# Kernel optimization log

Measured on AMD Instinct MI355X. Metric: run time of the kernel, lower is better.

## Reference

```python
import jax, jax.numpy as jnp
import numpy as np

T_GRID = 2048  # static grid size (= density * data range 128)
EPS = 1e-8


def rbf(x1, x2, ls, os_):
    # x1: [B,N,1], x2: [B,M,1] -> [B,N,M]; gpytorch ScaleKernel(RBFKernel())
    d2 = (x1 - jnp.swapaxes(x2, -1, -2)) ** 2
    return os_ * jnp.exp(-0.5 * d2 / (ls * ls))


def conv1d(x, w, b):
    # x: [B,C,T], w: [O,I,5], pad 2 -> same length
    y = jax.lax.conv_general_dilated(x, w, (1,), [(2, 2)],
                                     dimension_numbers=('NCH', 'OIH', 'NCH'))
    return y + b[None, :, None]


def setup_inputs() -> dict:
    key = jax.random.key(0)
    ks = jax.random.split(key, 12)
    B, Nc, Nt = 16, 2048, 2048
    xc = jax.random.uniform(ks[0], (B, Nc, 1), jnp.float32) * 128.0
    yc = jax.random.normal(ks[1], (B, Nc, 1), jnp.float32)
    xt = jax.random.uniform(ks[2], (B, Nt, 1), jnp.float32) * 128.0
    ln2 = float(np.log(2.0))  # softplus(0), gpytorch default raw param init
    params = {
        'ls_psi': jnp.float32(ln2), 'os_psi': jnp.float32(ln2),
        'ls_rho': jnp.float32(ln2), 'os_rho': jnp.float32(ln2),
        'w1': jax.random.normal(ks[3], (16, 3, 5), jnp.float32) * 0.2,
        'b1': jnp.zeros((16,), jnp.float32),
        'w2': jax.random.normal(ks[4], (32, 16, 5), jnp.float32) * 0.1,
        'b2': jnp.zeros((32,), jnp.float32),
        'w3': jax.random.normal(ks[5], (16, 32, 5), jnp.float32) * 0.1,
        'b3': jnp.zeros((16,), jnp.float32),
        'w4': jax.random.normal(ks[6], (2, 16, 5), jnp.float32) * 0.1,
        'b4': jnp.zeros((2,), jnp.float32),
    }
    return {'xc': xc, 'yc': yc, 'xt': xt, **params}


def reference(xc, yc, xt, ls_psi, os_psi, ls_rho, os_rho,
              w1, b1, w2, b2, w3, b3, w4, b4):
    B = xc.shape[0]
    lower = jnp.minimum(xc.min(), xt.min())
    upper = jnp.maximum(xc.max(), xt.max())
    t = jnp.linspace(lower, upper, T_GRID)                      # [T]
    t = jnp.broadcast_to(t[None, :, None], (B, T_GRID, 1))      # [B,T,1]

    # SetConv encoder: h = psi(t, xc) @ phi(yc), phi = [y^0, y^1]
    Kt = rbf(t, xc, ls_psi, os_psi)                             # [B,T,Nc]
    phi = jnp.concatenate([jnp.ones_like(yc), yc], -1)          # [B,Nc,2]
    h = jnp.matmul(Kt, phi)                                     # [B,T,2]
    h0, h1 = h[..., :1], h[..., 1:]
    h1 = h1 / (h0 + EPS)
    rep = jnp.concatenate([t, h0, h1], -1).swapaxes(-1, -2)     # [B,3,T]

    # small Conv1d decoder stack
    f = jax.nn.relu(conv1d(rep, w1, b1))
    f = jax.nn.relu(conv1d(f, w2, b2))
    f = jax.nn.relu(conv1d(f, w3, b3))
    f = conv1d(f, w4, b4).swapaxes(-1, -2)                      # [B,T,2]
    f_mu, f_sigma = f[..., :1], f[..., 1:]

    # SetConv decoder onto targets
    Kr = rbf(xt, t, ls_rho, os_rho)                             # [B,Nt,T]
    mu = jnp.matmul(Kr, f_mu)                                   # [B,Nt,1]
    sigma = jnp.matmul(Kr, jax.nn.softplus(f_sigma))            # [B,Nt,1]
    return jnp.concatenate([mu, sigma], -1)                     # [B,Nt,2]
```

## Files before the change

### kernel.cpp

```cpp
#include <hip/hip_runtime.h>
#include <math.h>

#define T_GRID 2048
#define NC 2048
#define NT 2048
#define BATCH 16
#define XCUT 28.0f
#define TILE 128
#define SW 144
#define W 149
#define PCAP 768
#define NSB 32

__global__ __launch_bounds__(1024) void k_minmax(const float4* __restrict__ xc4,
                                                 const float4* __restrict__ xt4,
                                                 float* __restrict__ mm) {
    float4 va[8], vb[8];
    int tid = threadIdx.x;
#pragma unroll
    for (int k = 0; k < 8; k++) va[k] = xc4[tid + 1024 * k];
#pragma unroll
    for (int k = 0; k < 8; k++) vb[k] = xt4[tid + 1024 * k];
    float lo = 3.4e38f, hi = -3.4e38f;
#pragma unroll
    for (int k = 0; k < 8; k++) {
        lo = fminf(lo, fminf(fminf(va[k].x, va[k].y), fminf(va[k].z, va[k].w)));
        hi = fmaxf(hi, fmaxf(fmaxf(va[k].x, va[k].y), fmaxf(va[k].z, va[k].w)));
        lo = fminf(lo, fminf(fminf(vb[k].x, vb[k].y), fminf(vb[k].z, vb[k].w)));
        hi = fmaxf(hi, fmaxf(fmaxf(vb[k].x, vb[k].y), fmaxf(vb[k].z, vb[k].w)));
    }
    for (int off = 32; off; off >>= 1) {
        lo = fminf(lo, __shfl_down(lo, off));
        hi = fmaxf(hi, __shfl_down(hi, off));
    }
    __shared__ float slo[16], shi[16];
    int lane = tid & 63, wv = tid >> 6;
    if (lane == 0) { slo[wv] = lo; shi[wv] = hi; }
    __syncthreads();
    if (tid == 0) {
        for (int w = 1; w < 16; w++) { lo = fminf(lo, slo[w]); hi = fmaxf(hi, shi[w]); }
        mm[0] = lo; mm[1] = hi;
    }
}

__global__ __launch_bounds__(576) void k_fused(
        const float* __restrict__ xc, const float* __restrict__ yc,
        const float* __restrict__ ls_psi, const float* __restrict__ os_psi,
        const float* __restrict__ mm,
        const float* __restrict__ w1, const float* __restrict__ b1,
        const float* __restrict__ w2, const float* __restrict__ b2,
        const float* __restrict__ w3, const float* __restrict__ b3,
        const float* __restrict__ w4, const float* __restrict__ b4,
        float* __restrict__ f) {
    __shared__ float rep[3][W];
    __shared__ float L1s[16][W];
    __shared__ __align__(16) char pool[32 * W * 4];
    __shared__ float w1L[15][16];
    __shared__ float w2L[80][32];
    __shared__ float w3L[160][16];
    __shared__ float w4L[80][2];
    __shared__ float bL[66];

    float (*L2s)[W] = reinterpret_cast<float (*)[W]>(pool);
    float (*L3s)[W] = L1s;
    float*  px     = reinterpret_cast<float*>(pool);
    float*  py     = reinterpret_cast<float*>(pool + 3072);
    float2* part   = reinterpret_cast<float2*>(pool + 6144);
    int*    bstart = reinterpret_cast<int*>(pool + 10752);
    int*    curi   = reinterpret_cast<int*>(pool + 10896);

    int tid = threadIdx.x;
    int b = blockIdx.y;
    int gstart = blockIdx.x * TILE - 8;

    for (int idx = tid; idx < 240; idx += 576)  { int o = idx / 15,  r2 = idx % 15;  w1L[r2][o] = w1[idx]; }
    for (int idx = tid; idx < 2560; idx += 576) { int o = idx / 80,  r2 = idx % 80;  w2L[r2][o] = w2[idx]; }
    for (int idx = tid; idx < 2560; idx += 576) { int o = idx / 160, r2 = idx % 160; w3L[r2][o] = w3[idx]; }
    for (int idx = tid; idx < 160; idx += 576)  { int o = idx / 80,  r2 = idx % 80;  w4L[r2][o] = w4[idx]; }
    if (tid < 16) bL[tid] = b1[tid];
    if (tid < 32) bL[16 + tid] = b2[tid];
    if (tid < 16) bL[48 + tid] = b3[tid];
    if (tid < 2)  bL[64 + tid] = b4[tid];
    if (tid < 4) {
        int c = (tid < 2) ? tid : tid + SW;
        for (int r2 = 0; r2 < 3; r2++)  rep[r2][c] = 0.f;
        for (int r2 = 0; r2 < 16; r2++) L1s[r2][c] = 0.f;
    }

    float lower = mm[0], upper = mm[1];
    float step = (upper - lower) * (1.0f / (T_GRID - 1));
    float ls = ls_psi[0], os = os_psi[0];
    float c2 = -0.72134752044f / (ls * ls);
    float R = ls * sqrtf(XCUT);

    int g0 = max(gstart, 0), g1 = min(gstart + SW - 1, T_GRID - 1);
    float tmin = fmaf((float)g0, step, lower) - R;
    float tmax = fmaf((float)g1, step, lower) + R;
    float sbw_inv = (float)NSB / (tmax - tmin);

    if (tid < NSB + 1) bstart[tid] = 0;
    __syncthreads();
    float xv[4], yv[4];
    int bn[4];
    const float* xb = xc + b * NC;
    const float* yb = yc + b * NC;
#pragma unroll
    for (int k = 0; k < 4; k++) {
        int idx = tid + 576 * k;
        bn[k] = -1;
        if (idx < NC) {
            xv[k] = xb[idx];
            yv[k] = yb[idx];
            if ((xv[k] >= tmin) & (xv[k] <= tmax)) {
                bn[k] = min(NSB - 1, max(0, (int)((xv[k] - tmin) * sbw_inv)));
                atomicAdd(&bstart[bn[k]], 1);
            }
        }
    }
    __syncthreads();
    if (tid == 0) {
        int run = 0;
        for (int i = 0; i < NSB; i++) { int c = bstart[i]; bstart[i] = run; run += c; }
        bstart[NSB] = run;
    }
    __syncthreads();
    if (tid < NSB) curi[tid] = bstart[tid];
    __syncthreads();
#pragma unroll
    for (int k = 0; k < 4; k++) {
        if (bn[k] >= 0) {
            int pos = atomicAdd(&curi[bn[k]], 1);
            if (pos < PCAP) { px[pos] = xv[k]; py[pos] = yv[k]; }
        }
    }
    __syncthreads();

    {
        int p = tid >> 2, rr = tid & 3;
        int gp = gstart + p;
        bool pvalid = (gp >= 0 && gp < T_GRID);
        float t = fmaf((float)gp, step, lower);
        int s = 0, e = 0;
        if (pvalid) {
            int b0 = min(NSB - 1, max(0, (int)((t - R - tmin) * sbw_inv)));
            int b1 = min(NSB - 1, max(0, (int)((t + R - tmin) * sbw_inv)));
            s = bstart[b0];
            e = min(bstart[b1 + 1], PCAP);
        }
        float S0 = 0.f, S1 = 0.f;
        for (int j = s + rr; j < e; j += 4) {
            float xj = px[j], yj = py[j];
            float d = t - xj;
            float ev = exp2f(d * d * c2);
            S0 += ev;
            S1 = fmaf(ev, yj, S1);
        }
        part[rr * SW + p] = make_float2(S0, S1);
        __syncthreads();
        if (tid < SW) {
            float2 q0 = part[tid], q1 = part[tid + SW], q2 = part[tid + 2 * SW], q3 = part[tid + 3 * SW];
            float T0 = q0.x + q1.x + q2.x + q3.x;
            float T1 = q0.y + q1.y + q2.y + q3.y;
            int gp2 = gstart + tid;
            bool pv2 = (gp2 >= 0 && gp2 < T_GRID);
            float h0 = os * T0;
            float h1 = os * T1 / (h0 + 1e-8f);
            rep[0][tid + 2] = pv2 ? fmaf((float)gp2, step, lower) : 0.f;
            rep[1][tid + 2] = pv2 ? h0 : 0.f;
            rep[2][tid + 2] = pv2 ? h1 : 0.f;
        }
    }
    __syncthreads();

    {
        if (tid < 4) {
            int c = (tid < 2) ? tid : tid + SW;
            for (int r2 = 0; r2 < 32; r2++) L2s[r2][c] = 0.f;
        }
        int o = tid & 15, s0 = (tid >> 4) << 2;
        float acc[4];
        float bias = bL[o];
#pragma unroll
        for (int s = 0; s < 4; s++) acc[s] = bias;
        for (int i = 0; i < 3; i++) {
            float x[8];
#pragma unroll
            for (int j = 0; j < 8; j++) x[j] = rep[i][s0 + j];
#pragma unroll
            for (int k = 0; k < 5; k++) {
                float w = w1L[i * 5 + k][o];
#pragma unroll
                for (int s = 0; s < 4; s++) acc[s] = fmaf(x[s + k], w, acc[s]);
            }
        }
#pragma unroll
        for (int s = 0; s < 4; s++) {
            int p = s0 + s, gp = gstart + p;
            bool vv = (p >= 2 && p < SW - 2 && gp >= 0 && gp < T_GRID);
            L1s[o][p + 2] = vv ? fmaxf(acc[s], 0.f) : 0.f;
        }
    }
    __syncthreads();

    {
        int o = tid & 31, s0 = (tid >> 5) << 3;
        float acc[8];
        float bias = bL[16 + o];
#pragma unroll
        for (int s = 0; s < 8; s++) acc[s] = bias;
        for (int i = 0; i < 16; i++) {
            float x[12];
#pragma unroll
            for (int j = 0; j < 12; j++) x[j] = L1s[i][s0 + j];
#pragma unroll
            for (int k = 0; k < 5; k++) {
                float w = w2L[i * 5 + k][o];
#pragma unroll
                for (int s = 0; s < 8; s++) acc[s] = fmaf(x[s + k], w, acc[s]);
            }
        }
#pragma unroll
        for (int s = 0; s < 8; s++) {
            int p = s0 + s, gp = gstart + p;
            bool vv = (p >= 4 && p < SW - 4 && gp >= 0 && gp < T_GRID);
            L2s[o][p + 2] = vv ? fmaxf(acc[s], 0.f) : 0.f;
        }
    }
    __syncthreads();

    {
        int o = tid & 15, s0 = (tid >> 4) << 2;
        float acc[4];
        float bias = bL[48 + o];
#pragma unroll
        for (int s = 0; s < 4; s++) acc[s] = bias;
        for (int i = 0; i < 32; i++) {
            float x[8];
#pragma unroll
            for (int j = 0; j < 8; j++) x[j] = L2s[i][s0 + j];
#pragma unroll
            for (int k = 0; k < 5; k++) {
                float w = w3L[i * 5 + k][o];
#pragma unroll
                for (int s = 0; s < 4; s++) acc[s] = fmaf(x[s + k], w, acc[s]);
            }
        }
#pragma unroll
        for (int s = 0; s < 4; s++) {
            int p = s0 + s, gp = gstart + p;
            bool vv = (p >= 6 && p < SW - 6 && gp >= 0 && gp < T_GRID);
            L3s[o][p + 2] = vv ? fmaxf(acc[s], 0.f) : 0.f;
        }
    }
    __syncthreads();

    if (tid < 256) {
        int o = tid & 1, po = tid >> 1;
        float a = bL[64 + o];
        for (int i = 0; i < 16; i++) {
#pragma unroll
            for (int k = 0; k < 5; k++) {
                a = fmaf(L3s[i][po + 8 + k], w4L[i * 5 + k][o], a);
            }
        }
        int gp = blockIdx.x * TILE + po;
        if (o) {
            float sp = fmaxf(a, 0.f) + log1pf(expf(-fabsf(a)));
            f[2 * (b * T_GRID + gp) + 1] = sp;
        } else {
            f[2 * (b * T_GRID + gp)] = a;
        }
    }
}

__global__ __launch_bounds__(256) void k_out(const float* __restrict__ xt,
                                             const float* __restrict__ ls_rho,
                                             const float* __restrict__ os_rho,
                                             const float* __restrict__ mm,
                                             const float2* __restrict__ f,
                                             float2* __restrict__ out) {
    __shared__ float smx[T_GRID];
    __shared__ float ssg[T_GRID];
    __shared__ float2 part[256];
    int b = blockIdx.y, tid = threadIdx.x;
    int it = blockIdx.x * 64 + (tid & 63);
    int r = tid >> 6;
    float lower = mm[0], upper = mm[1];
    float step = (upper - lower) * (1.0f / (T_GRID - 1));
    float invstep = 1.0f / step;
    float ls = ls_rho[0], os = os_rho[0];
    float c2 = -0.72134752044f / (ls * ls);
    float R = ls * sqrtf(XCUT);
    float x = xt[b * NT + it];

    const float2* fb = f + b * T_GRID;
    for (int k = tid; k < T_GRID; k += 256) {
        float2 v = fb[k];
        smx[k] = v.x; ssg[k] = v.y;
    }
    __syncthreads();

    int j0 = max(0, (int)floorf((x - R - lower) * invstep));
    int j1 = min(T_GRID - 1, (int)ceilf((x + R - lower) * invstep));

    float Smu = 0.f, Ssg = 0.f;
    float jf = (float)(j0 + r);
    for (int j = j0 + r; j <= j1; j += 4) {
        float d = x - fmaf(jf, step, lower);
        float e = exp2f(d * d * c2);
        Smu = fmaf(e, smx[j], Smu);
        Ssg = fmaf(e, ssg[j], Ssg);
        jf += 4.0f;
    }
    part[tid] = make_float2(Smu, Ssg);
    __syncthreads();
    if (r == 0) {
#pragma unroll
        for (int q = 64; q < 256; q += 64) {
            float2 pp = part[tid + q];
            Smu += pp.x; Ssg += pp.y;
        }
        out[b * NT + it] = make_float2(os * Smu, os * Ssg);
    }
}

extern "C" void kernel_launch(void* const* d_in, const int* in_sizes, int n_in,
                              void* d_out, int out_size, void* d_ws, size_t ws_size,
                              hipStream_t stream) {
    const float* xc = (const float*)d_in[0];
    const float* yc = (const float*)d_in[1];
    const float* xt = (const float*)d_in[2];
    const float* ls_psi = (const float*)d_in[3];
    const float* os_psi = (const float*)d_in[4];
    const float* ls_rho = (const float*)d_in[5];
    const float* os_rho = (const float*)d_in[6];
    const float* w1 = (const float*)d_in[7];
    const float* b1 = (const float*)d_in[8];
    const float* w2 = (const float*)d_in[9];
    const float* b2 = (const float*)d_in[10];
    const float* w3 = (const float*)d_in[11];
    const float* b3 = (const float*)d_in[12];
    const float* w4 = (const float*)d_in[13];
    const float* b4 = (const float*)d_in[14];

    char* ws = (char*)d_ws;
    float* mm = (float*)ws;
    float* f  = (float*)(ws + 64);

    k_minmax<<<dim3(1), dim3(1024), 0, stream>>>((const float4*)xc, (const float4*)xt, mm);

    k_fused<<<dim3(T_GRID / TILE, BATCH), dim3(576), 0, stream>>>(
        xc, yc, ls_psi, os_psi, mm,
        w1, b1, w2, b2, w3, b3, w4, b4, f);

    k_out<<<dim3(NT / 64, BATCH), dim3(256), 0, stream>>>(
        xt, ls_rho, os_rho, mm, (const float2*)f, (float2*)d_out);
}
```

Baseline: 109.6 us.

## Fuse all three kernels into one persistent kernel with grid barriers

Replaces the min/max, fused encoder+conv, and output kernels with a single 256-block kernel that uses software grid barriers on a workspace counter. The min/max is distributed across blocks with atomicMin/Max on order-preserving mapped floats, and the output stage reuses the same blocks with 512 active threads. This removes two kernel launch gaps and the serial single-block reduction, at the risk of barrier spin overhead and reliance on all 256 blocks being co-resident.

```diff
diff --git a/kernel.cpp b/kernel.cpp
--- a/kernel.cpp
+++ b/kernel.cpp
@@ -11,47 +11,40 @@
 #define W 149
 #define PCAP 768
 #define NSB 32
-
-__global__ __launch_bounds__(1024) void k_minmax(const float4* __restrict__ xc4,
-                                                 const float4* __restrict__ xt4,
-                                                 float* __restrict__ mm) {
-    float4 va[8], vb[8];
-    int tid = threadIdx.x;
-#pragma unroll
-    for (int k = 0; k < 8; k++) va[k] = xc4[tid + 1024 * k];
-#pragma unroll
-    for (int k = 0; k < 8; k++) vb[k] = xt4[tid + 1024 * k];
-    float lo = 3.4e38f, hi = -3.4e38f;
-#pragma unroll
-    for (int k = 0; k < 8; k++) {
-        lo = fminf(lo, fminf(fminf(va[k].x, va[k].y), fminf(va[k].z, va[k].w)));
-        hi = fmaxf(hi, fmaxf(fmaxf(va[k].x, va[k].y), fmaxf(va[k].z, va[k].w)));
-        lo = fminf(lo, fminf(fminf(vb[k].x, vb[k].y), fminf(vb[k].z, vb[k].w)));
-        hi = fmaxf(hi, fmaxf(fmaxf(vb[k].x, vb[k].y), fmaxf(vb[k].z, vb[k].w)));
-    }
-    for (int off = 32; off; off >>= 1) {
-        lo = fminf(lo, __shfl_down(lo, off));
-        hi = fmaxf(hi, __shfl_down(hi, off));
-    }
-    __shared__ float slo[16], shi[16];
-    int lane = tid & 63, wv = tid >> 6;
-    if (lane == 0) { slo[wv] = lo; shi[wv] = hi; }
+#define NBLK 256u
+#define MAGIC 0x1234ABCDu
+
+__device__ __forceinline__ unsigned mapf(float x) {
+    unsigned b = __float_as_uint(x);
+    return (b & 0x80000000u) ? ~b : (b | 0x80000000u);
+}
+__device__ __forceinline__ float unmapf(unsigned u) {
+    return (u & 0x80000000u) ? __uint_as_float(u & 0x7fffffffu) : __uint_as_float(~u);
+}
+
+__device__ __forceinline__ void gbar(unsigned* ctr) {
     __syncthreads();
-    if (tid == 0) {
-        for (int w = 1; w < 16; w++) { lo = fminf(lo, slo[w]); hi = fmaxf(hi, shi[w]); }
-        mm[0] = lo; mm[1] = hi;
-    }
-}
-
-__global__ __launch_bounds__(576) void k_fused(
+    if (threadIdx.x == 0) {
+        __threadfence();
+        __hip_atomic_fetch_add(ctr, 1u, __ATOMIC_RELEASE, __HIP_MEMORY_SCOPE_AGENT);
+        while (__hip_atomic_load(ctr, __ATOMIC_ACQUIRE, __HIP_MEMORY_SCOPE_AGENT) < NBLK)
+            __builtin_amdgcn_s_sleep(1);
+        __threadfence();
+    }
+    __syncthreads();
+}
+
+__global__ __launch_bounds__(576) void k_all(
         const float* __restrict__ xc, const float* __restrict__ yc,
+        const float* __restrict__ xt,
         const float* __restrict__ ls_psi, const float* __restrict__ os_psi,
-        const float* __restrict__ mm,
+        const float* __restrict__ ls_rho, const float* __restrict__ os_rho,
         const float* __restrict__ w1, const float* __restrict__ b1,
         const float* __restrict__ w2, const float* __restrict__ b2,
         const float* __restrict__ w3, const float* __restrict__ b3,
         const float* __restrict__ w4, const float* __restrict__ b4,
-        float* __restrict__ f) {
+        unsigned* __restrict__ syncv, float* __restrict__ f,
+        float2* __restrict__ out) {
     __shared__ float rep[3][W];
     __shared__ float L1s[16][W];
     __shared__ __align__(16) char pool[32 * W * 4];
@@ -70,8 +63,10 @@
     int*    curi   = reinterpret_cast<int*>(pool + 10896);
 
     int tid = threadIdx.x;
-    int b = blockIdx.y;
-    int gstart = blockIdx.x * TILE - 8;
+    int bid = blockIdx.x;
+    int b = bid >> 4;
+    int j = bid & 15;
+    int gstart = j * TILE - 8;
 
     for (int idx = tid; idx < 240; idx += 576)  { int o = idx / 15,  r2 = idx % 15;  w1L[r2][o] = w1[idx]; }
     for (int idx = tid; idx < 2560; idx += 576) { int o = idx / 80,  r2 = idx % 80;  w2L[r2][o] = w2[idx]; }
@@ -87,241 +82,276 @@
         for (int r2 = 0; r2 < 16; r2++) L1s[r2][c] = 0.f;
     }
 
-    float lower = mm[0], upper = mm[1];
+    float lo = 3.4e38f, hi = -3.4e38f;
+    if (tid < 64) {
+        const float4* p4 = (tid < 32) ? ((const float4*)xc + bid * 32 + tid)
+                                      : ((const float4*)xt + bid * 32 + (tid - 32));
+        float4 v = *p4;
+        lo = fminf(fminf(v.x, v.y), fminf(v.z, v.w));
+        hi = fmaxf(fmaxf(v.x, v.y), fmaxf(v.z, v.w));
+    }
+
+    if (tid == 0) {
+        if (bid == 0) {
+            __hip_atomic_store(&syncv[1], 0u, __ATOMIC_RELAXED, __HIP_MEMORY_SCOPE_AGENT);
+            __hip_atomic_store(&syncv[2], 0u, __ATOMIC_RELAXED, __HIP_MEMORY_SCOPE_AGENT);
+            __hip_atomic_store(&syncv[3], 0u, __ATOMIC_RELAXED, __HIP_MEMORY_SCOPE_AGENT);
+            __hip_atomic_store(&syncv[4], 0xFFFFFFFFu, __ATOMIC_RELAXED, __HIP_MEMORY_SCOPE_AGENT);
+            __hip_atomic_store(&syncv[5], 0u, __ATOMIC_RELAXED, __HIP_MEMORY_SCOPE_AGENT);
+            __hip_atomic_store(&syncv[0], MAGIC, __ATOMIC_RELEASE, __HIP_MEMORY_SCOPE_AGENT);
+        }
+        while (__hip_atomic_load(&syncv[0], __ATOMIC_ACQUIRE, __HIP_MEMORY_SCOPE_AGENT) != MAGIC)
+            __builtin_amdgcn_s_sleep(1);
+    }
+    __syncthreads();
+
+    if (tid < 64) {
+        for (int off = 32; off; off >>= 1) {
+            lo = fminf(lo, __shfl_down(lo, off));
+            hi = fmaxf(hi, __shfl_down(hi, off));
+        }
+        if (tid == 0) {
+            atomicMin(&syncv[4], mapf(lo));
+            atomicMax(&syncv[5], mapf(hi));
+        }
+    }
+    gbar(&syncv[1]);
+
+    float lower = unmapf(__hip_atomic_load(&syncv[4], __ATOMIC_RELAXED, __HIP_MEMORY_SCOPE_AGENT));
+    float upper = unmapf(__hip_atomic_load(&syncv[5], __ATOMIC_RELAXED, __HIP_MEMORY_SCOPE_AGENT));
     float step = (upper - lower) * (1.0f / (T_GRID - 1));
-    float ls = ls_psi[0], os = os_psi[0];
-    float c2 = -0.72134752044f / (ls * ls);
-    float R = ls * sqrtf(XCUT);
-
-    int g0 = max(gstart, 0), g1 = min(gstart + SW - 1, T_GRID - 1);
-    float tmin = fmaf((float)g0, step, lower) - R;
-    float tmax = fmaf((float)g1, step, lower) + R;
-    float sbw_inv = (float)NSB / (tmax - tmin);
-
-    if (tid < NSB + 1) bstart[tid] = 0;
-    __syncthreads();
-    float xv[4], yv[4];
-    int bn[4];
-    const float* xb = xc + b * NC;
-    const float* yb = yc + b * NC;
-#pragma unroll
-    for (int k = 0; k < 4; k++) {
-        int idx = tid + 576 * k;
-        bn[k] = -1;
-        if (idx < NC) {
-            xv[k] = xb[idx];
-            yv[k] = yb[idx];
-            if ((xv[k] >= tmin) & (xv[k] <= tmax)) {
-                bn[k] = min(NSB - 1, max(0, (int)((xv[k] - tmin) * sbw_inv)));
-                atomicAdd(&bstart[bn[k]], 1);
-            }
-        }
-    }
-    __syncthreads();
-    if (tid == 0) {
-        int run = 0;
-        for (int i = 0; i < NSB; i++) { int c = bstart[i]; bstart[i] = run; run += c; }
-        bstart[NSB] = run;
-    }
-    __syncthreads();
-    if (tid < NSB) curi[tid] = bstart[tid];
-    __syncthreads();
-#pragma unroll
-    for (int k = 0; k < 4; k++) {
-        if (bn[k] >= 0) {
-            int pos = atomicAdd(&curi[bn[k]], 1);
-            if (pos < PCAP) { px[pos] = xv[k]; py[pos] = yv[k]; }
-        }
-    }
-    __syncthreads();
 
     {
-        int p = tid >> 2, rr = tid & 3;
-        int gp = gstart + p;
-        bool pvalid = (gp >= 0 && gp < T_GRID);
-        float t = fmaf((float)gp, step, lower);
-        int s = 0, e = 0;
-        if (pvalid) {
-            int b0 = min(NSB - 1, max(0, (int)((t - R - tmin) * sbw_inv)));
-            int b1 = min(NSB - 1, max(0, (int)((t + R - tmin) * sbw_inv)));
-            s = bstart[b0];
-            e = min(bstart[b1 + 1], PCAP);
-        }
-        float S0 = 0.f, S1 = 0.f;
-        for (int j = s + rr; j < e; j += 4) {
-            float xj = px[j], yj = py[j];
-            float d = t - xj;
-            float ev = exp2f(d * d * c2);
-            S0 += ev;
-            S1 = fmaf(ev, yj, S1);
-        }
-        part[rr * SW + p] = make_float2(S0, S1);
-        __syncthreads();
-        if (tid < SW) {
-            float2 q0 = part[tid], q1 = part[tid + SW], q2 = part[tid + 2 * SW], q3 = part[tid + 3 * SW];
-            float T0 = q0.x + q1.x + q2.x + q3.x;
-            float T1 = q0.y + q1.y + q2.y + q3.y;
-            int gp2 = gstart + tid;
-            bool pv2 = (gp2 >= 0 && gp2 < T_GRID);
-            float h0 = os * T0;
-            float h1 = os * T1 / (h0 + 1e-8f);
-            rep[0][tid + 2] = pv2 ? fmaf((float)gp2, step, lower) : 0.f;
-            rep[1][tid + 2] = pv2 ? h0 : 0.f;
-            rep[2][tid + 2] = pv2 ? h1 : 0.f;
-        }
-    }
-    __syncthreads();
+        float ls = ls_psi[0], os = os_psi[0];
+        float c2 = -0.72134752044f / (ls * ls);
+        float R = ls * sqrtf(XCUT);
+
+        int g0 = max(gstart, 0), g1 = min(gstart + SW - 1, T_GRID - 1);
+        float tmin = fmaf((float)g0, step, lower) - R;
+        float tmax = fmaf((float)g1, step, lower) + R;
+        float sbw_inv = (float)NSB / (tmax - tmin);
+
+        if (tid < NSB + 1) bstart[tid] = 0;
+        __syncthreads();
+        float xv[4], yv[4];
+        int bn[4];
+        const float* xb = xc + b * NC;
+        const float* yb = yc + b * NC;
+#pragma unroll
+        for (int k = 0; k < 4; k++) {
+            int idx = tid + 576 * k;
+            bn[k] = -1;
+            if (idx < NC) {
+                xv[k] = xb[idx];
+                yv[k] = yb[idx];
+                if ((xv[k] >= tmin) & (xv[k] <= tmax)) {
+                    bn[k] = min(NSB - 1, max(0, (int)((xv[k] - tmin) * sbw_inv)));
+                    atomicAdd(&bstart[bn[k]], 1);
+                }
+            }
+        }
+        __syncthreads();
+        if (tid == 0) {
+            int run = 0;
+            for (int i = 0; i < NSB; i++) { int c = bstart[i]; bstart[i] = run; run += c; }
+            bstart[NSB] = run;
+        }
+        __syncthreads();
+        if (tid < NSB) curi[tid] = bstart[tid];
+        __syncthreads();
+#pragma unroll
+        for (int k = 0; k < 4; k++) {
+            if (bn[k] >= 0) {
+                int pos = atomicAdd(&curi[bn[k]], 1);
+                if (pos < PCAP) { px[pos] = xv[k]; py[pos] = yv[k]; }
+            }
+        }
+        __syncthreads();
+
+        {
+            int p = tid >> 2, rr = tid & 3;
+            int gp = gstart + p;
+            bool pvalid = (gp >= 0 && gp < T_GRID);
+            float t = fmaf((float)gp, step, lower);
+            int s = 0, e = 0;
+            if (pvalid) {
+                int b0 = min(NSB - 1, max(0, (int)((t - R - tmin) * sbw_inv)));
+                int b1i = min(NSB - 1, max(0, (int)((t + R - tmin) * sbw_inv)));
+                s = bstart[b0];
+                e = min(bstart[b1i + 1], PCAP);
+            }
+            float S0 = 0.f, S1 = 0.f;
+            for (int jj = s + rr; jj < e; jj += 4) {
+                float xj = px[jj], yj = py[jj];
+                float d = t - xj;
+                float ev = exp2f(d * d * c2);
+                S0 += ev;
+                S1 = fmaf(ev, yj, S1);
+            }
+            part[rr * SW + p] = make_float2(S0, S1);
+            __syncthreads();
+            if (tid < SW) {
+                float2 q0 = part[tid], q1 = part[tid + SW], q2 = part[tid + 2 * SW], q3 = part[tid + 3 * SW];
+                float T0 = q0.x + q1.x + q2.x + q3.x;
+                float T1 = q0.y + q1.y + q2.y + q3.y;
+                int gp2 = gstart + tid;
+                bool pv2 = (gp2 >= 0 && gp2 < T_GRID);
+                float h0 = os * T0;
+                float h1 = os * T1 / (h0 + 1e-8f);
+                rep[0][tid + 2] = pv2 ? fmaf((float)gp2, step, lower) : 0.f;
+                rep[1][tid + 2] = pv2 ? h0 : 0.f;
+                rep[2][tid + 2] = pv2 ? h1 : 0.f;
+            }
+        }
+        __syncthreads();
+
+        {
+            if (tid < 4) {
+                int c = (tid < 2) ? tid : tid + SW;
+                for (int r2 = 0; r2 < 32; r2++) L2s[r2][c] = 0.f;
+            }
+            int o = tid & 15, s0 = (tid >> 4) << 2;
+            float acc[4];
+            float bias = bL[o];
+#pragma unroll
+            for (int s = 0; s < 4; s++) acc[s] = bias;
+            for (int i = 0; i < 3; i++) {
+                float x[8];
+#pragma unroll
+                for (int jj = 0; jj < 8; jj++) x[jj] = rep[i][s0 + jj];
+#pragma unroll
+                for (int k = 0; k < 5; k++) {
+                    float w = w1L[i * 5 + k][o];
+#pragma unroll
+                    for (int s = 0; s < 4; s++) acc[s] = fmaf(x[s + k], w, acc[s]);
+                }
+            }
+#pragma unroll
+            for (int s = 0; s < 4; s++) {
+                int p = s0 + s, gp = gstart + p;
+                bool vv = (p >= 2 && p < SW - 2 && gp >= 0 && gp < T_GRID);
+                L1s[o][p + 2] = vv ? fmaxf(acc[s], 0.f) : 0.f;
+            }
+        }
+        __syncthreads();
+
+        {
+            int o = tid & 31, s0 = (tid >> 5) << 3;
+            float acc[8];
+            float bias = bL[16 + o];
+#pragma unroll
+            for (int s = 0; s < 8; s++) acc[s] = bias;
+            for (int i = 0; i < 16; i++) {
+                float x[12];
+#pragma unroll
+                for (int jj = 0; jj < 12; jj++) x[jj] = L1s[i][s0 + jj];
+#pragma unroll
+                for (int k = 0; k < 5; k++) {
+                    float w = w2L[i * 5 + k][o];
+#pragma unroll
+                    for (int s = 0; s < 8; s++) acc[s] = fmaf(x[s + k], w, acc[s]);
+                }
+            }
+#pragma unroll
+            for (int s = 0; s < 8; s++) {
+                int p = s0 + s, gp = gstart + p;
+                bool vv = (p >= 4 && p < SW - 4 && gp >= 0 && gp < T_GRID);
+                L2s[o][p + 2] = vv ? fmaxf(acc[s], 0.f) : 0.f;
+            }
+        }
+        __syncthreads();
+
+        {
+            int o = tid & 15, s0 = (tid >> 4) << 2;
+            float acc[4];
+            float bias = bL[48 + o];
+#pragma unroll
+            for (int s = 0; s < 4; s++) acc[s] = bias;
+            for (int i = 0; i < 32; i++) {
+                float x[8];
+#pragma unroll
+                for (int jj = 0; jj < 8; jj++) x[jj] = L2s[i][s0 + jj];
+#pragma unroll
+                for (int k = 0; k < 5; k++) {
+                    float w = w3L[i * 5 + k][o];
+#pragma unroll
+                    for (int s = 0; s < 4; s++) acc[s] = fmaf(x[s + k], w, acc[s]);
+                }
+            }
+#pragma unroll
+            for (int s = 0; s < 4; s++) {
+                int p = s0 + s, gp = gstart + p;
+                bool vv = (p >= 6 && p < SW - 6 && gp >= 0 && gp < T_GRID);
+                L3s[o][p + 2] = vv ? fmaxf(acc[s], 0.f) : 0.f;
+            }
+        }
+        __syncthreads();
+
+        if (tid < 256) {
+            int o = tid & 1, po = tid >> 1;
+            float a = bL[64 + o];
+            for (int i = 0; i < 16; i++) {
+#pragma unroll
+                for (int k = 0; k < 5; k++) {
+                    a = fmaf(L3s[i][po + 8 + k], w4L[i * 5 + k][o], a);
+                }
+            }
+            int gp = j * TILE + po;
+            if (o) {
+                float sp = fmaxf(a, 0.f) + log1pf(expf(-fabsf(a)));
+                f[2 * (b * T_GRID + gp) + 1] = sp;
+            } else {
+                f[2 * (b * T_GRID + gp)] = a;
+            }
+        }
+    }
+    gbar(&syncv[2]);
 
     {
-        if (tid < 4) {
-            int c = (tid < 2) ? tid : tid + SW;
-            for (int r2 = 0; r2 < 32; r2++) L2s[r2][c] = 0.f;
-        }
-        int o = tid & 15, s0 = (tid >> 4) << 2;
-        float acc[4];
-        float bias = bL[o];
-#pragma unroll
-        for (int s = 0; s < 4; s++) acc[s] = bias;
-        for (int i = 0; i < 3; i++) {
-            float x[8];
-#pragma unroll
-            for (int j = 0; j < 8; j++) x[j] = rep[i][s0 + j];
-#pragma unroll
-            for (int k = 0; k < 5; k++) {
-                float w = w1L[i * 5 + k][o];
-#pragma unroll
-                for (int s = 0; s < 4; s++) acc[s] = fmaf(x[s + k], w, acc[s]);
-            }
-        }
-#pragma unroll
-        for (int s = 0; s < 4; s++) {
-            int p = s0 + s, gp = gstart + p;
-            bool vv = (p >= 2 && p < SW - 2 && gp >= 0 && gp < T_GRID);
-            L1s[o][p + 2] = vv ? fmaxf(acc[s], 0.f) : 0.f;
-        }
-    }
-    __syncthreads();
-
-    {
-        int o = tid & 31, s0 = (tid >> 5) << 3;
-        float acc[8];
-        float bias = bL[16 + o];
-#pragma unroll
-        for (int s = 0; s < 8; s++) acc[s] = bias;
-        for (int i = 0; i < 16; i++) {
-            float x[12];
-#pragma unroll
-            for (int j = 0; j < 12; j++) x[j] = L1s[i][s0 + j];
-#pragma unroll
-            for (int k = 0; k < 5; k++) {
-                float w = w2L[i * 5 + k][o];
-#pragma unroll
-                for (int s = 0; s < 8; s++) acc[s] = fmaf(x[s + k], w, acc[s]);
-            }
-        }
-#pragma unroll
-        for (int s = 0; s < 8; s++) {
-            int p = s0 + s, gp = gstart + p;
-            bool vv = (p >= 4 && p < SW - 4 && gp >= 0 && gp < T_GRID);
-            L2s[o][p + 2] = vv ? fmaxf(acc[s], 0.f) : 0.f;
-        }
-    }
-    __syncthreads();
-
-    {
-        int o = tid & 15, s0 = (tid >> 4) << 2;
-        float acc[4];
-        float bias = bL[48 + o];
-#pragma unroll
-        for (int s = 0; s < 4; s++) acc[s] = bias;
-        for (int i = 0; i < 32; i++) {
-            float x[8];
-#pragma unroll
-            for (int j = 0; j < 8; j++) x[j] = L2s[i][s0 + j];
-#pragma unroll
-            for (int k = 0; k < 5; k++) {
-                float w = w3L[i * 5 + k][o];
-#pragma unroll
-                for (int s = 0; s < 4; s++) acc[s] = fmaf(x[s + k], w, acc[s]);
-            }
-        }
-#pragma unroll
-        for (int s = 0; s < 4; s++) {
-            int p = s0 + s, gp = gstart + p;
-            bool vv = (p >= 6 && p < SW - 6 && gp >= 0 && gp < T_GRID);
-            L3s[o][p + 2] = vv ? fmaxf(acc[s], 0.f) : 0.f;
-        }
-    }
-    __syncthreads();
-
-    if (tid < 256) {
-        int o = tid & 1, po = tid >> 1;
-        float a = bL[64 + o];
-        for (int i = 0; i < 16; i++) {
-#pragma unroll
-            for (int k = 0; k < 5; k++) {
-                a = fmaf(L3s[i][po + 8 + k], w4L[i * 5 + k][o], a);
-            }
-        }
-        int gp = blockIdx.x * TILE + po;
-        if (o) {
-            float sp = fmaxf(a, 0.f) + log1pf(expf(-fabsf(a)));
-            f[2 * (b * T_GRID + gp) + 1] = sp;
-        } else {
-            f[2 * (b * T_GRID + gp)] = a;
-        }
-    }
-}
-
-__global__ __launch_bounds__(256) void k_out(const float* __restrict__ xt,
-                                             const float* __restrict__ ls_rho,
-                                             const float* __restrict__ os_rho,
-                                             const float* __restrict__ mm,
-                                             const float2* __restrict__ f,
-                                             float2* __restrict__ out) {
-    __shared__ float smx[T_GRID];
-    __shared__ float ssg[T_GRID];
-    __shared__ float2 part[256];
-    int b = blockIdx.y, tid = threadIdx.x;
-    int it = blockIdx.x * 64 + (tid & 63);
-    int r = tid >> 6;
-    float lower = mm[0], upper = mm[1];
-    float step = (upper - lower) * (1.0f / (T_GRID - 1));
-    float invstep = 1.0f / step;
-    float ls = ls_rho[0], os = os_rho[0];
-    float c2 = -0.72134752044f / (ls * ls);
-    float R = ls * sqrtf(XCUT);
-    float x = xt[b * NT + it];
-
-    const float2* fb = f + b * T_GRID;
-    for (int k = tid; k < T_GRID; k += 256) {
-        float2 v = fb[k];
-        smx[k] = v.x; ssg[k] = v.y;
-    }
-    __syncthreads();
-
-    int j0 = max(0, (int)floorf((x - R - lower) * invstep));
-    int j1 = min(T_GRID - 1, (int)ceilf((x + R - lower) * invstep));
-
-    float Smu = 0.f, Ssg = 0.f;
-    float jf = (float)(j0 + r);
-    for (int j = j0 + r; j <= j1; j += 4) {
-        float d = x - fmaf(jf, step, lower);
-        float e = exp2f(d * d * c2);
-        Smu = fmaf(e, smx[j], Smu);
-        Ssg = fmaf(e, ssg[j], Ssg);
-        jf += 4.0f;
-    }
-    part[tid] = make_float2(Smu, Ssg);
-    __syncthreads();
-    if (r == 0) {
-#pragma unroll
-        for (int q = 64; q < 256; q += 64) {
-            float2 pp = part[tid + q];
-            Smu += pp.x; Ssg += pp.y;
-        }
-        out[b * NT + it] = make_float2(os * Smu, os * Ssg);
-    }
+        float* smx = reinterpret_cast<float*>(pool);
+        float* ssg = reinterpret_cast<float*>(pool + 8192);
+        float2* part3 = reinterpret_cast<float2*>(&L1s[0][0]);
+
+        float ls = ls_rho[0], os = os_rho[0];
+        float c2 = -0.72134752044f / (ls * ls);
+        float R = ls * sqrtf(XCUT);
+        float invstep = 1.0f / step;
+
+        const float2* fb = (const float2*)f + b * T_GRID;
+        for (int k = tid; k < T_GRID; k += 576) {
+            float2 v = fb[k];
+            smx[k] = v.x; ssg[k] = v.y;
+        }
+        __syncthreads();
+
+        float Smu = 0.f, Ssg = 0.f;
+        int q = tid >> 2, rr = tid & 3;
+        if (tid < 512) {
+            float x = xt[b * NT + j * 128 + q];
+            int j0 = max(0, (int)floorf((x - R - lower) * invstep));
+            int j1 = min(T_GRID - 1, (int)ceilf((x + R - lower) * invstep));
+            float jf = (float)(j0 + rr);
+            for (int jj = j0 + rr; jj <= j1; jj += 4) {
+                float d = x - fmaf(jf, step, lower);
+                float e = exp2f(d * d * c2);
+                Smu = fmaf(e, smx[jj], Smu);
+                Ssg = fmaf(e, ssg[jj], Ssg);
+                jf += 4.0f;
+            }
+            part3[rr * 128 + q] = make_float2(Smu, Ssg);
+        }
+        __syncthreads();
+        if (tid < 128) {
+            float2 p0 = part3[tid], p1 = part3[128 + tid], p2 = part3[256 + tid], p3 = part3[384 + tid];
+            float sm = p0.x + p1.x + p2.x + p3.x;
+            float sg = p0.y + p1.y + p2.y + p3.y;
+            out[b * NT + j * 128 + tid] = make_float2(os * sm, os * sg);
+        }
+    }
+
+    gbar(&syncv[3]);
+    if (bid == 0 && tid == 0)
+        __hip_atomic_store(&syncv[0], 0u, __ATOMIC_RELAXED, __HIP_MEMORY_SCOPE_AGENT);
 }
 
 extern "C" void kernel_launch(void* const* d_in, const int* in_sizes, int n_in,
@@ -344,15 +374,11 @@
     const float* b4 = (const float*)d_in[14];
 
     char* ws = (char*)d_ws;
-    float* mm = (float*)ws;
-    float* f  = (float*)(ws + 64);
-
-    k_minmax<<<dim3(1), dim3(1024), 0, stream>>>((const float4*)xc, (const float4*)xt, mm);
-
-    k_fused<<<dim3(T_GRID / TILE, BATCH), dim3(576), 0, stream>>>(
-        xc, yc, ls_psi, os_psi, mm,
-        w1, b1, w2, b2, w3, b3, w4, b4, f);
-
-    k_out<<<dim3(NT / 64, BATCH), dim3(256), 0, stream>>>(
-        xt, ls_rho, os_rho, mm, (const float2*)f, (float2*)d_out);
-}
+    unsigned* syncv = (unsigned*)ws;
+    float* f = (float*)(ws + 256);
+
+    k_all<<<dim3(NBLK), dim3(576), 0, stream>>>(
+        xc, yc, xt, ls_psi, os_psi, ls_rho, os_rho,
+        w1, b1, w2, b2, w3, b3, w4, b4,
+        syncv, f, (float2*)d_out);
+}
```

After: 172.4 us. +57.3%, slower.

## Fold global min/max reduction into fused kernel, drop separate minmax launch

Applied to the files above, without the earlier changes.

Removes the single-block min/max kernel and has every block of the fused kernel redundantly reduce all xc and xt values (256 KB) to get the grid bounds, with block (0,0) writing them out for the output kernel. This trades a serial one-block launch and its dependency for redundant global reads across 256 blocks, which will mostly hit in cache. It also vectorizes the per-batch xc load to float4 and loads yc only for in-range points. An extra barrier is added in the third conv layer because L3s aliases L1s.

```diff
diff --git a/kernel.cpp b/kernel.cpp
--- a/kernel.cpp
+++ b/kernel.cpp
@@ -12,46 +12,15 @@
 #define PCAP 768
 #define NSB 32
 
-__global__ __launch_bounds__(1024) void k_minmax(const float4* __restrict__ xc4,
-                                                 const float4* __restrict__ xt4,
-                                                 float* __restrict__ mm) {
-    float4 va[8], vb[8];
-    int tid = threadIdx.x;
-#pragma unroll
-    for (int k = 0; k < 8; k++) va[k] = xc4[tid + 1024 * k];
-#pragma unroll
-    for (int k = 0; k < 8; k++) vb[k] = xt4[tid + 1024 * k];
-    float lo = 3.4e38f, hi = -3.4e38f;
-#pragma unroll
-    for (int k = 0; k < 8; k++) {
-        lo = fminf(lo, fminf(fminf(va[k].x, va[k].y), fminf(va[k].z, va[k].w)));
-        hi = fmaxf(hi, fmaxf(fmaxf(va[k].x, va[k].y), fmaxf(va[k].z, va[k].w)));
-        lo = fminf(lo, fminf(fminf(vb[k].x, vb[k].y), fminf(vb[k].z, vb[k].w)));
-        hi = fmaxf(hi, fmaxf(fmaxf(vb[k].x, vb[k].y), fmaxf(vb[k].z, vb[k].w)));
-    }
-    for (int off = 32; off; off >>= 1) {
-        lo = fminf(lo, __shfl_down(lo, off));
-        hi = fmaxf(hi, __shfl_down(hi, off));
-    }
-    __shared__ float slo[16], shi[16];
-    int lane = tid & 63, wv = tid >> 6;
-    if (lane == 0) { slo[wv] = lo; shi[wv] = hi; }
-    __syncthreads();
-    if (tid == 0) {
-        for (int w = 1; w < 16; w++) { lo = fminf(lo, slo[w]); hi = fmaxf(hi, shi[w]); }
-        mm[0] = lo; mm[1] = hi;
-    }
-}
-
 __global__ __launch_bounds__(576) void k_fused(
         const float* __restrict__ xc, const float* __restrict__ yc,
+        const float4* __restrict__ xc4, const float4* __restrict__ xt4,
         const float* __restrict__ ls_psi, const float* __restrict__ os_psi,
-        const float* __restrict__ mm,
         const float* __restrict__ w1, const float* __restrict__ b1,
         const float* __restrict__ w2, const float* __restrict__ b2,
         const float* __restrict__ w3, const float* __restrict__ b3,
         const float* __restrict__ w4, const float* __restrict__ b4,
-        float* __restrict__ f) {
+        float* __restrict__ mm, float* __restrict__ f) {
     __shared__ float rep[3][W];
     __shared__ float L1s[16][W];
     __shared__ __align__(16) char pool[32 * W * 4];
@@ -60,6 +29,7 @@
     __shared__ float w3L[160][16];
     __shared__ float w4L[80][2];
     __shared__ float bL[66];
+    __shared__ float slo[9], shi[9];
 
     float (*L2s)[W] = reinterpret_cast<float (*)[W]>(pool);
     float (*L3s)[W] = L1s;
@@ -87,7 +57,33 @@
         for (int r2 = 0; r2 < 16; r2++) L1s[r2][c] = 0.f;
     }
 
-    float lower = mm[0], upper = mm[1];
+    float lo = 3.4e38f, hi = -3.4e38f;
+    for (int i = tid; i < BATCH * NC / 4; i += 576) {
+        float4 v = xc4[i];
+        lo = fminf(lo, fminf(fminf(v.x, v.y), fminf(v.z, v.w)));
+        hi = fmaxf(hi, fmaxf(fmaxf(v.x, v.y), fmaxf(v.z, v.w)));
+    }
+    for (int i = tid; i < BATCH * NT / 4; i += 576) {
+        float4 v = xt4[i];
+        lo = fminf(lo, fminf(fminf(v.x, v.y), fminf(v.z, v.w)));
+        hi = fmaxf(hi, fmaxf(fmaxf(v.x, v.y), fmaxf(v.z, v.w)));
+    }
+    for (int off = 32; off; off >>= 1) {
+        lo = fminf(lo, __shfl_down(lo, off));
+        hi = fmaxf(hi, __shfl_down(hi, off));
+    }
+    {
+        int lane = tid & 63, wv = tid >> 6;
+        if (lane == 0) { slo[wv] = lo; shi[wv] = hi; }
+    }
+    if (tid < NSB + 1) bstart[tid] = 0;
+    __syncthreads();
+    lo = slo[0]; hi = shi[0];
+#pragma unroll
+    for (int w2i = 1; w2i < 9; w2i++) { lo = fminf(lo, slo[w2i]); hi = fmaxf(hi, shi[w2i]); }
+    float lower = lo, upper = hi;
+    if (blockIdx.x == 0 && blockIdx.y == 0 && tid == 0) { mm[0] = lower; mm[1] = upper; }
+
     float step = (upper - lower) * (1.0f / (T_GRID - 1));
     float ls = ls_psi[0], os = os_psi[0];
     float c2 = -0.72134752044f / (ls * ls);
@@ -98,24 +94,24 @@
     float tmax = fmaf((float)g1, step, lower) + R;
     float sbw_inv = (float)NSB / (tmax - tmin);
 
-    if (tid < NSB + 1) bstart[tid] = 0;
-    __syncthreads();
     float xv[4], yv[4];
     int bn[4];
-    const float* xb = xc + b * NC;
     const float* yb = yc + b * NC;
-#pragma unroll
-    for (int k = 0; k < 4; k++) {
-        int idx = tid + 576 * k;
-        bn[k] = -1;
-        if (idx < NC) {
-            xv[k] = xb[idx];
-            yv[k] = yb[idx];
+    if (tid < 512) {
+        float4 v = ((const float4*)(xc + b * NC))[tid];
+        xv[0] = v.x; xv[1] = v.y; xv[2] = v.z; xv[3] = v.w;
+#pragma unroll
+        for (int k = 0; k < 4; k++) {
+            bn[k] = -1;
             if ((xv[k] >= tmin) & (xv[k] <= tmax)) {
                 bn[k] = min(NSB - 1, max(0, (int)((xv[k] - tmin) * sbw_inv)));
+                yv[k] = yb[4 * tid + k];
                 atomicAdd(&bstart[bn[k]], 1);
             }
         }
+    } else {
+#pragma unroll
+        for (int k = 0; k < 4; k++) bn[k] = -1;
     }
     __syncthreads();
     if (tid == 0) {
@@ -143,9 +139,9 @@
         int s = 0, e = 0;
         if (pvalid) {
             int b0 = min(NSB - 1, max(0, (int)((t - R - tmin) * sbw_inv)));
-            int b1 = min(NSB - 1, max(0, (int)((t + R - tmin) * sbw_inv)));
+            int b1i = min(NSB - 1, max(0, (int)((t + R - tmin) * sbw_inv)));
             s = bstart[b0];
-            e = min(bstart[b1 + 1], PCAP);
+            e = min(bstart[b1i + 1], PCAP);
         }
         float S0 = 0.f, S1 = 0.f;
         for (int j = s + rr; j < e; j += 4) {
@@ -245,6 +241,7 @@
                 for (int s = 0; s < 4; s++) acc[s] = fmaf(x[s + k], w, acc[s]);
             }
         }
+        __syncthreads();
 #pragma unroll
         for (int s = 0; s < 4; s++) {
             int p = s0 + s, gp = gstart + p;
@@ -345,13 +342,11 @@
 
     char* ws = (char*)d_ws;
     float* mm = (float*)ws;
-    float* f  = (float*)(ws + 64);
-
-    k_minmax<<<dim3(1), dim3(1024), 0, stream>>>((const float4*)xc, (const float4*)xt, mm);
+    float* f  = (float*)(ws + 256);
 
     k_fused<<<dim3(T_GRID / TILE, BATCH), dim3(576), 0, stream>>>(
-        xc, yc, ls_psi, os_psi, mm,
-        w1, b1, w2, b2, w3, b3, w4, b4, f);
+        xc, yc, (const float4*)xc, (const float4*)xt, ls_psi, os_psi,
+        w1, b1, w2, b2, w3, b3, w4, b4, mm, f);
 
     k_out<<<dim3(NT / 64, BATCH), dim3(256), 0, stream>>>(
         xt, ls_rho, os_rho, mm, (const float2*)f, (float2*)d_out);
```

Result: slower. 112.7 us (+2.8%).
